# Optimization experiments

Measured on AMD Instinct MI355X. Metric: run time of the kernel, lower is better.

## Reference

```python
import jax, jax.numpy as jnp
import numpy as np

V, D, NH, L, HID, E, K = 32000, 1024, 16, 2, 2048, 8, 2
B, S = 2, 1024
HD = D // NH
EPS = 1e-6
ROPE_BASE = 10000.0


def setup_inputs() -> dict:
    key = jax.random.key(0)
    ks = jax.random.split(key, 12)
    s = 0.02
    return {
        "tokens": jax.random.randint(ks[0], (B, S), 0, V),
        "embed": jax.random.normal(ks[1], (V, D), jnp.float32) * s,
        "attn_norm_w": jnp.ones((L, D), jnp.float32),
        "wq": jax.random.normal(ks[2], (L, D, D), jnp.float32) * s,
        "wk": jax.random.normal(ks[3], (L, D, D), jnp.float32) * s,
        "wv": jax.random.normal(ks[4], (L, D, D), jnp.float32) * s,
        "wo": jax.random.normal(ks[5], (L, D, D), jnp.float32) * s,
        "moe_norm_w": jnp.ones((L, D), jnp.float32),
        "router_w": jax.random.normal(ks[6], (L, E, D), jnp.float32) * s,
        "w1": jax.random.normal(ks[7], (L, E, D, HID), jnp.float32) * s,
        "w2": jax.random.normal(ks[8], (L, E, HID, D), jnp.float32) * s,
        "w3": jax.random.normal(ks[9], (L, E, D, HID), jnp.float32) * s,
        "final_norm_w": jnp.ones((D,), jnp.float32),
    }


def rmsnorm(x, w):
    var = jnp.mean(jnp.square(x), axis=-1, keepdims=True)
    return x * jax.lax.rsqrt(var + EPS) * w


def rope(x):  # x: [B, S, NH, HD], rotate-half convention
    half = HD // 2
    inv = ROPE_BASE ** (-jnp.arange(half, dtype=jnp.float32) / half)
    ang = jnp.arange(x.shape[1], dtype=jnp.float32)[:, None] * inv[None, :]  # [S, half]
    cos = jnp.cos(ang)[None, :, None, :]
    sin = jnp.sin(ang)[None, :, None, :]
    x1, x2 = x[..., :half], x[..., half:]
    return jnp.concatenate([x1 * cos - x2 * sin, x1 * sin + x2 * cos], axis=-1)


def attention(x, wq, wk, wv, wo):
    q = (x @ wq).reshape(B, S, NH, HD)
    k = (x @ wk).reshape(B, S, NH, HD)
    v = (x @ wv).reshape(B, S, NH, HD)
    q, k = rope(q), rope(k)
    scores = jnp.einsum("bqhd,bkhd->bhqk", q, k) / jnp.sqrt(jnp.float32(HD))
    mask = jnp.tril(jnp.ones((S, S), bool))
    scores = jnp.where(mask[None, None], scores, jnp.finfo(scores.dtype).min)
    attn = jax.nn.softmax(scores, axis=-1)
    ctx = jnp.einsum("bhqk,bkhd->bqhd", attn, v).reshape(B, S, D)
    return ctx @ wo


def moe(x, router_w, w1, w2, w3):
    flat = x.reshape(-1, D)                      # [T, D]
    T = flat.shape[0]
    logits = flat @ router_w.T                   # [T, E]
    topv, topi = jax.lax.top_k(logits, K)
    topw = jax.nn.softmax(topv, axis=-1)         # softmax over selected logits
    gates = jnp.zeros((T, E), flat.dtype).at[jnp.arange(T)[:, None], topi].set(topw)
    out = jnp.zeros_like(flat)
    for e in range(E):  # small fixed expert count; gates are exact-sparse so math == dispatch path
        y = (jax.nn.silu(flat @ w1[e]) * (flat @ w3[e])) @ w2[e]
        out = out + y * gates[:, e:e + 1]
    return out.reshape(x.shape)


def reference(tokens, embed, attn_norm_w, wq, wk, wv, wo, moe_norm_w,
              router_w, w1, w2, w3, final_norm_w):
    x = embed[tokens]  # [B, S, D]
    for l in range(L):
        x = x + attention(rmsnorm(x, attn_norm_w[l]), wq[l], wk[l], wv[l], wo[l])
        x = x + moe(rmsnorm(x, moe_norm_w[l]), router_w[l], w1[l], w2[l], w3[l])
    x = rmsnorm(x, final_norm_w)
    return x @ embed.T  # tied logits [B, S, V]
```

## Files before the change

kernel.cpp:

```cpp
#include <hip/hip_runtime.h>
#include <math.h>

typedef unsigned short u16;
typedef unsigned int u32;
typedef __attribute__((ext_vector_type(8))) short bf16x8;
typedef __attribute__((ext_vector_type(4))) float f32x4;

#define TOK 2048
#define SEQ 1024
#define DM 1024
#define NEXP 8
#define VOCAB 32000
#define NL 2
#define SLOTS 5120
#define APAD 40

__device__ __forceinline__ float bf2f(u16 v) {
  u32 u = ((u32)v) << 16; float f; __builtin_memcpy(&f, &u, 4); return f;
}
__device__ __forceinline__ u16 f2bf(float f) {
  u32 u; __builtin_memcpy(&u, &f, 4);
  u += 0x7fffu + ((u >> 16) & 1u);
  return (u16)(u >> 16);
}
__device__ __forceinline__ void split8(const float* v, u16* hi, u16* lo) {
#pragma unroll
  for (int j = 0; j < 8; j++) {
    hi[j] = f2bf(v[j]);
    lo[j] = f2bf(v[j] - bf2f(hi[j]));
  }
}

__global__ __launch_bounds__(256) void k_f2bf(const float* __restrict__ in,
                                              u16* __restrict__ out, long n4) {
  long i = (long)blockIdx.x * 256 + threadIdx.x;
  long stride = (long)gridDim.x * 256;
  for (; i < n4; i += stride) {
    float4 v = ((const float4*)in)[i];
    ushort4 o;
    o.x = f2bf(v.x); o.y = f2bf(v.y); o.z = f2bf(v.z); o.w = f2bf(v.w);
    ((ushort4*)out)[i] = o;
  }
}

__device__ __forceinline__ void norm_emit_hl(float4 v, const float* __restrict__ w,
    u16* __restrict__ ohi, u16* __restrict__ olo, int t) {
  float ss = v.x * v.x + v.y * v.y + v.z * v.z + v.w * v.w;
  for (int off = 32; off; off >>= 1) ss += __shfl_xor(ss, off);
  __shared__ float red[4];
  if ((threadIdx.x & 63) == 0) red[threadIdx.x >> 6] = ss;
  __syncthreads();
  float tot = red[0] + red[1] + red[2] + red[3];
  float sc = rsqrtf(tot * (1.0f / 1024.0f) + 1e-6f);
  float4 wv = ((const float4*)w)[threadIdx.x];
  float o[4] = {v.x * sc * wv.x, v.y * sc * wv.y, v.z * sc * wv.z, v.w * sc * wv.w};
  ushort4 hi, lo;
  hi.x = f2bf(o[0]); lo.x = f2bf(o[0] - bf2f(hi.x));
  hi.y = f2bf(o[1]); lo.y = f2bf(o[1] - bf2f(hi.y));
  hi.z = f2bf(o[2]); lo.z = f2bf(o[2] - bf2f(hi.z));
  hi.w = f2bf(o[3]); lo.w = f2bf(o[3] - bf2f(hi.w));
  ((ushort4*)(ohi + (long)t * DM))[threadIdx.x] = hi;
  ((ushort4*)(olo + (long)t * DM))[threadIdx.x] = lo;
}
__device__ __forceinline__ void norm_emit_b(float4 v, const float* __restrict__ w,
    u16* __restrict__ out, int t) {
  float ss = v.x * v.x + v.y * v.y + v.z * v.z + v.w * v.w;
  for (int off = 32; off; off >>= 1) ss += __shfl_xor(ss, off);
  __shared__ float red[4];
  if ((threadIdx.x & 63) == 0) red[threadIdx.x >> 6] = ss;
  __syncthreads();
  float tot = red[0] + red[1] + red[2] + red[3];
  float sc = rsqrtf(tot * (1.0f / 1024.0f) + 1e-6f);
  float4 wv = ((const float4*)w)[threadIdx.x];
  ushort4 o;
  o.x = f2bf(v.x * sc * wv.x); o.y = f2bf(v.y * sc * wv.y);
  o.z = f2bf(v.z * sc * wv.z); o.w = f2bf(v.w * sc * wv.w);
  ((ushort4*)(out + (long)t * DM))[threadIdx.x] = o;
}

__global__ __launch_bounds__(256) void k_gather_norm(const int* __restrict__ tok,
    const float* __restrict__ embed, const float* __restrict__ w,
    float* __restrict__ x, u16* __restrict__ ohi, u16* __restrict__ olo) {
  int t = blockIdx.x;
  float4 v = ((const float4*)(embed + (long)tok[t] * DM))[threadIdx.x];
  ((float4*)(x + (long)t * DM))[threadIdx.x] = v;
  norm_emit_hl(v, w, ohi, olo, t);
}

__global__ __launch_bounds__(256) void k_rmsnorm_hl(const float* __restrict__ x,
    const float* __restrict__ w, u16* __restrict__ ohi, u16* __restrict__ olo) {
  int t = blockIdx.x;
  float4 v = ((const float4*)(x + (long)t * DM))[threadIdx.x];
  norm_emit_hl(v, w, ohi, olo, t);
}

#define KP 72
#define VP 40
#define PP 36
__global__ __launch_bounds__(256) void k_attn(const float* __restrict__ qkv,
    u16* __restrict__ chi, u16* __restrict__ clo) {
  __shared__ u16 Ksh[32 * KP], Ksl[32 * KP];
  __shared__ u16 Vsh[64 * VP], Vsl[64 * VP];
  __shared__ float Ps[4][16 * PP];
  int bid = blockIdx.x;
  int xcd = bid & 7, r = bid >> 3;
  int bh = xcd * 4 + (r >> 4);
  int qt = 15 - (r & 15);
  int b = bh >> 4, h = bh & 15;
  int tid = threadIdx.x, w = tid >> 6, lane = tid & 63;
  int lrow = lane & 15, lgrp = lane >> 4;
  int q0 = qt * 64;
  long qrow = (long)(b * SEQ + q0 + w * 16 + lrow);
  bf16x8 qh[2], ql[2];
#pragma unroll
  for (int dsl = 0; dsl < 2; dsl++) {
    const float* src = qkv + qrow * 3072 + h * 64 + dsl * 32 + lgrp * 8;
    float v[8];
    *(float4*)v = *(const float4*)src;
    *(float4*)(v + 4) = *(const float4*)(src + 4);
    u16 hi[8], lo[8];
    split8(v, hi, lo);
    qh[dsl] = *(bf16x8*)hi; ql[dsl] = *(bf16x8*)lo;
  }
  f32x4 cacc[4] = {};
  float mst[4], lst[4];
#pragma unroll
  for (int j = 0; j < 4; j++) { mst[j] = -__builtin_inff(); lst[j] = 0.0f; }
  int srow = tid >> 3, dchunk = (tid & 7) * 8;
  for (int s0 = 0; s0 < q0 + 64; s0 += 32) {
    long kvrow = (long)(b * SEQ + s0 + srow) * 3072 + h * 64;
    {
      const float* ksrc = qkv + kvrow + 1024 + dchunk;
      float v[8];
      *(float4*)v = *(const float4*)ksrc;
      *(float4*)(v + 4) = *(const float4*)(ksrc + 4);
#pragma unroll
      for (int j = 0; j < 8; j++) {
        u16 hi = f2bf(v[j]);
        Ksh[srow * KP + dchunk + j] = hi;
        Ksl[srow * KP + dchunk + j] = f2bf(v[j] - bf2f(hi));
      }
      const float* vsrc = qkv + kvrow + 2048 + dchunk;
      *(float4*)v = *(const float4*)vsrc;
      *(float4*)(v + 4) = *(const float4*)(vsrc + 4);
#pragma unroll
      for (int j = 0; j < 8; j++) {
        u16 hi = f2bf(v[j]);
        Vsh[(dchunk + j) * VP + srow] = hi;
        Vsl[(dchunk + j) * VP + srow] = f2bf(v[j] - bf2f(hi));
      }
    }
    __syncthreads();
    f32x4 sacc[2] = {};
#pragma unroll
    for (int sf = 0; sf < 2; sf++)
#pragma unroll
      for (int dsl = 0; dsl < 2; dsl++) {
        bf16x8 kh = *(const bf16x8*)(Ksh + (sf * 16 + lrow) * KP + dsl * 32 + lgrp * 8);
        bf16x8 kl = *(const bf16x8*)(Ksl + (sf * 16 + lrow) * KP + dsl * 32 + lgrp * 8);
        sacc[sf] = __builtin_amdgcn_mfma_f32_16x16x32_bf16(qh[dsl], kh, sacc[sf], 0, 0, 0);
        sacc[sf] = __builtin_amdgcn_mfma_f32_16x16x32_bf16(qh[dsl], kl, sacc[sf], 0, 0, 0);
        sacc[sf] = __builtin_amdgcn_mfma_f32_16x16x32_bf16(ql[dsl], kh, sacc[sf], 0, 0, 0);
      }
#pragma unroll
    for (int sf = 0; sf < 2; sf++)
#pragma unroll
      for (int j = 0; j < 4; j++) {
        int col = s0 + sf * 16 + lrow;
        int row = q0 + w * 16 + lgrp * 4 + j;
        float v = sacc[sf][j] * 0.125f;
        sacc[sf][j] = (col <= row) ? v : -1e30f;
      }
    float fac[4];
#pragma unroll
    for (int j = 0; j < 4; j++) {
      float mx = fmaxf(sacc[0][j], sacc[1][j]);
      for (int off = 1; off < 16; off <<= 1) mx = fmaxf(mx, __shfl_xor(mx, off));
      float mnew = fmaxf(mst[j], mx);
      float f = __expf(mst[j] - mnew);
      mst[j] = mnew;
      float p0 = __expf(sacc[0][j] - mnew);
      float p1 = __expf(sacc[1][j] - mnew);
      sacc[0][j] = p0; sacc[1][j] = p1;
      float ps = p0 + p1;
      for (int off = 1; off < 16; off <<= 1) ps += __shfl_xor(ps, off);
      lst[j] = lst[j] * f + ps;
      fac[j] = f;
    }
#pragma unroll
    for (int n = 0; n < 4; n++)
#pragma unroll
      for (int j = 0; j < 4; j++) cacc[n][j] *= fac[j];
#pragma unroll
    for (int sf = 0; sf < 2; sf++)
#pragma unroll
      for (int j = 0; j < 4; j++)
        Ps[w][(lgrp * 4 + j) * PP + sf * 16 + lrow] = sacc[sf][j];
    float pv[8];
#pragma unroll
    for (int j = 0; j < 8; j++) pv[j] = Ps[w][lrow * PP + lgrp * 8 + j];
    u16 phi[8], plo[8];
    split8(pv, phi, plo);
    bf16x8 ph = *(bf16x8*)phi, pl = *(bf16x8*)plo;
#pragma unroll
    for (int n = 0; n < 4; n++) {
      bf16x8 vh = *(const bf16x8*)(Vsh + (n * 16 + lrow) * VP + lgrp * 8);
      bf16x8 vl = *(const bf16x8*)(Vsl + (n * 16 + lrow) * VP + lgrp * 8);
      cacc[n] = __builtin_amdgcn_mfma_f32_16x16x32_bf16(ph, vh, cacc[n], 0, 0, 0);
      cacc[n] = __builtin_amdgcn_mfma_f32_16x16x32_bf16(ph, vl, cacc[n], 0, 0, 0);
      cacc[n] = __builtin_amdgcn_mfma_f32_16x16x32_bf16(pl, vh, cacc[n], 0, 0, 0);
    }
    __syncthreads();
  }
#pragma unroll
  for (int n = 0; n < 4; n++)
#pragma unroll
    for (int j = 0; j < 4; j++) {
      long t = (long)(b * SEQ + q0 + w * 16 + lgrp * 4 + j);
      float v = cacc[n][j] / lst[j];
      u16 hv = f2bf(v);
      chi[t * DM + h * 64 + n * 16 + lrow] = hv;
      clo[t * DM + h * 64 + n * 16 + lrow] = f2bf(v - bf2f(hv));
    }
}


__device__ __forceinline__ void stageB_tr(const float* __restrict__ B, int ldb,
    int k0, int n0, u16* Bh, u16* Bl, int tid, int split) {
#pragma unroll
  for (int ph = 0; ph < 2; ph++) {
    int c = tid + 256 * ph;
    int nr = c & 127;
    int ks = c >> 7;
    const float* src = B + (long)(k0 + ks * 8) * ldb + n0 + nr;
    float v[8];
#pragma unroll
    for (int j = 0; j < 8; j++) v[j] = src[(long)j * ldb];
    u16 hi[8];
#pragma unroll
    for (int j = 0; j < 8; j++) hi[j] = f2bf(v[j]);
    *(uint4*)(Bh + nr * APAD + ks * 8) = *(uint4*)hi;
    if (split) {
      u16 lo[8];
#pragma unroll
      for (int j = 0; j < 8; j++) lo[j] = f2bf(v[j] - bf2f(hi[j]));
      *(uint4*)(Bl + nr * APAD + ks * 8) = *(uint4*)lo;
    }
  }
}

__device__ __forceinline__ void stageA_cp(const u16* __restrict__ Ahi,
    const u16* __restrict__ Alo, long ldk, long m0, int k0,
    u16* Ah, u16* Al, int tid, int split) {
#pragma unroll
  for (int ph = 0; ph < 2; ph++) {
    int c = tid + 256 * ph;
    int row = c >> 2, kc = c & 3;
    long off = (m0 + row) * ldk + k0 + kc * 8;
    *(uint4*)(Ah + row * APAD + kc * 8) = *(const uint4*)(Ahi + off);
    if (split) *(uint4*)(Al + row * APAD + kc * 8) = *(const uint4*)(Alo + off);
  }
}

__global__ __launch_bounds__(256) void k_wo(
    const u16* __restrict__ Ahi, const u16* __restrict__ Alo,
    const float* __restrict__ B, float* __restrict__ C) {
  __shared__ u16 Ah[128 * APAD], Al[128 * APAD], Bh[128 * APAD], Bl[128 * APAD];
  int bid = blockIdx.x;
  int n0 = (bid & 7) * 128;
  int m0 = (bid >> 3) * 128;
  int tid = threadIdx.x, lane = tid & 63, w = tid >> 6;
  int wr = w >> 1, wc = w & 1, lrow = lane & 15, lgrp = lane >> 4;
  f32x4 acc[4][4] = {};
  for (int k0 = 0; k0 < 1024; k0 += 32) {
    stageA_cp(Ahi, Alo, DM, m0, k0, Ah, Al, tid, 1);
    stageB_tr(B, 1024, k0, n0, Bh, Bl, tid, 1);
    __syncthreads();
    bf16x8 ah[4], bh[4], al[4], bl[4];
#pragma unroll
    for (int i = 0; i < 4; i++) {
      ah[i] = *(const bf16x8*)(Ah + (wr * 64 + i * 16 + lrow) * APAD + lgrp * 8);
      al[i] = *(const bf16x8*)(Al + (wr * 64 + i * 16 + lrow) * APAD + lgrp * 8);
      bh[i] = *(const bf16x8*)(Bh + (wc * 64 + i * 16 + lrow) * APAD + lgrp * 8);
      bl[i] = *(const bf16x8*)(Bl + (wc * 64 + i * 16 + lrow) * APAD + lgrp * 8);
    }
#pragma unroll
    for (int i = 0; i < 4; i++)
#pragma unroll
      for (int j = 0; j < 4; j++) {
        acc[i][j] = __builtin_amdgcn_mfma_f32_16x16x32_bf16(ah[i], bh[j], acc[i][j], 0, 0, 0);
        acc[i][j] = __builtin_amdgcn_mfma_f32_16x16x32_bf16(ah[i], bl[j], acc[i][j], 0, 0, 0);
        acc[i][j] = __builtin_amdgcn_mfma_f32_16x16x32_bf16(al[i], bh[j], acc[i][j], 0, 0, 0);
      }
    __syncthreads();
  }
#pragma unroll
  for (int i = 0; i < 4; i++)
#pragma unroll
    for (int j = 0; j < 4; j++) {
      int col = n0 + wc * 64 + j * 16 + lrow;
#pragma unroll
      for (int jj = 0; jj < 4; jj++) {
        int r = m0 + wr * 64 + i * 16 + lgrp * 4 + jj;
        C[(long)r * DM + col] += acc[i][j][jj];
      }
    }
}

__global__ __launch_bounds__(256) void k_gemm_qkv(
    const u16* __restrict__ Ahi, const u16* __restrict__ Alo,
    const float* __restrict__ Bq, const float* __restrict__ Bk,
    const float* __restrict__ Bv, float* __restrict__ C) {
  __shared__ u16 Ah[128 * APAD], Al[128 * APAD], Bh[128 * APAD], Bl[128 * APAD];
  int bid = blockIdx.x;
  int xcd = bid & 7, r = bid >> 3;
  int nb = xcd * 3 + r / 16;
  int m0 = (r & 15) * 128;
  const float* B = (nb < 8) ? Bq : (nb < 16) ? Bk : Bv;
  int bn0 = (nb & 7) * 128;
  int tid = threadIdx.x, lane = tid & 63, w = tid >> 6;
  int wr = w >> 1, wc = w & 1, lrow = lane & 15, lgrp = lane >> 4;
  f32x4 acc[4][4] = {};
  for (int k0 = 0; k0 < 1024; k0 += 32) {
    stageA_cp(Ahi, Alo, DM, m0, k0, Ah, Al, tid, 1);
    stageB_tr(B, 1024, k0, bn0, Bh, Bl, tid, 1);
    __syncthreads();
    bf16x8 ah[4], bh[4], al[4], bl[4];
#pragma unroll
    for (int i = 0; i < 4; i++) {
      ah[i] = *(const bf16x8*)(Ah + (wr * 64 + i * 16 + lrow) * APAD + lgrp * 8);
      al[i] = *(const bf16x8*)(Al + (wr * 64 + i * 16 + lrow) * APAD + lgrp * 8);
      bh[i] = *(const bf16x8*)(Bh + (wc * 64 + i * 16 + lrow) * APAD + lgrp * 8);
      bl[i] = *(const bf16x8*)(Bl + (wc * 64 + i * 16 + lrow) * APAD + lgrp * 8);
    }
#pragma unroll
    for (int i = 0; i < 4; i++)
#pragma unroll
      for (int j = 0; j < 4; j++) {
        acc[i][j] = __builtin_amdgcn_mfma_f32_16x16x32_bf16(ah[i], bh[j], acc[i][j], 0, 0, 0);
        acc[i][j] = __builtin_amdgcn_mfma_f32_16x16x32_bf16(ah[i], bl[j], acc[i][j], 0, 0, 0);
        acc[i][j] = __builtin_amdgcn_mfma_f32_16x16x32_bf16(al[i], bh[j], acc[i][j], 0, 0, 0);
      }
    __syncthreads();
  }
  if (nb < 16) {
    float inv1 = exp2f((float)lrow * (-13.287712379549449f / 32.0f));
    float inv2 = exp2f((float)(lrow + 16) * (-13.287712379549449f / 32.0f));
#pragma unroll
    for (int i = 0; i < 4; i++)
#pragma unroll
      for (int jj = 0; jj < 4; jj++) {
        int rr = m0 + wr * 64 + i * 16 + lgrp * 4 + jj;
        float s = (float)(rr & (SEQ - 1));
        float sn1, cs1, sn2, cs2;
        sincosf(s * inv1, &sn1, &cs1);
        sincosf(s * inv2, &sn2, &cs2);
        float q1 = acc[i][0][jj], q2 = acc[i][2][jj];
        acc[i][0][jj] = q1 * cs1 - q2 * sn1;
        acc[i][2][jj] = q1 * sn1 + q2 * cs1;
        float p1 = acc[i][1][jj], p2 = acc[i][3][jj];
        acc[i][1][jj] = p1 * cs2 - p2 * sn2;
        acc[i][3][jj] = p1 * sn2 + p2 * cs2;
      }
  }
#pragma unroll
  for (int i = 0; i < 4; i++)
#pragma unroll
    for (int j = 0; j < 4; j++) {
      int col = nb * 128 + wc * 64 + j * 16 + lrow;
#pragma unroll
      for (int jj = 0; jj < 4; jj++) {
        int rr = m0 + wr * 64 + i * 16 + lgrp * 4 + jj;
        C[(long)rr * 3072 + col] = acc[i][j][jj];
      }
    }
}

template <int SPLIT>
__global__ __launch_bounds__(256) void k_w13(
    const u16* __restrict__ Ahi, const u16* __restrict__ Alo,
    const float* __restrict__ W1, const float* __restrict__ W3,
    const int* __restrict__ lists, const int* __restrict__ counts,
    const int* __restrict__ aoff,
    float* __restrict__ h13) {
  int bid = blockIdx.x;
  int xcd = bid & 7, r = bid >> 3;
  int nb = xcd * 4 + r / 40;
  int m0 = (r % 40) * 128;
  int e = -1;
#pragma unroll
  for (int i = 0; i < NEXP; i++)
    if (m0 >= aoff[i] && m0 < aoff[i + 1]) e = i;
  if (e < 0) return;
  int lr0 = m0 - aoff[e];
  int Mc = counts[e];
  if (lr0 >= Mc) return;
  const float* B = ((nb < 16) ? W1 : W3) + (size_t)e * 1024 * 2048;
  int bn0 = (nb & 15) * 128;
  const int* lst = lists + e * TOK;
  __shared__ u16 Ah[128 * APAD], Bh[128 * APAD];
  __shared__ u16 Al[SPLIT ? 128 * APAD : 1], Bl[SPLIT ? 128 * APAD : 1];
  int tid = threadIdx.x, lane = tid & 63, w = tid >> 6;
  int wr = w >> 1, wc = w & 1, lrow = lane & 15, lgrp = lane >> 4;
  f32x4 acc[4][4] = {};
  for (int k0 = 0; k0 < 1024; k0 += 32) {
#pragma unroll
    for (int ph = 0; ph < 2; ph++) {
      int c = tid + 256 * ph;
      int row = c >> 2, kc = c & 3;
      uint4 vh = make_uint4(0, 0, 0, 0), vl = make_uint4(0, 0, 0, 0);
      if (lr0 + row < Mc) {
        long off = (long)lst[lr0 + row] * DM + k0 + kc * 8;
        vh = *(const uint4*)(Ahi + off);
        if (SPLIT) vl = *(const uint4*)(Alo + off);
      }
      *(uint4*)(Ah + row * APAD + kc * 8) = vh;
      if (SPLIT) *(uint4*)(Al + row * APAD + kc * 8) = vl;
    }
    stageB_tr(B, 2048, k0, bn0, Bh, Bl, tid, SPLIT);
    __syncthreads();
    bf16x8 ah[4], bh[4];
#pragma unroll
    for (int i = 0; i < 4; i++) {
      ah[i] = *(const bf16x8*)(Ah + (wr * 64 + i * 16 + lrow) * APAD + lgrp * 8);
      bh[i] = *(const bf16x8*)(Bh + (wc * 64 + i * 16 + lrow) * APAD + lgrp * 8);
    }
#pragma unroll
    for (int i = 0; i < 4; i++)
#pragma unroll
      for (int j = 0; j < 4; j++)
        acc[i][j] = __builtin_amdgcn_mfma_f32_16x16x32_bf16(ah[i], bh[j], acc[i][j], 0, 0, 0);
    if (SPLIT) {
      bf16x8 al[4], bl[4];
#pragma unroll
      for (int i = 0; i < 4; i++) {
        al[i] = *(const bf16x8*)(Al + (wr * 64 + i * 16 + lrow) * APAD + lgrp * 8);
        bl[i] = *(const bf16x8*)(Bl + (wc * 64 + i * 16 + lrow) * APAD + lgrp * 8);
      }
#pragma unroll
      for (int i = 0; i < 4; i++)
#pragma unroll
        for (int j = 0; j < 4; j++) {
          acc[i][j] = __builtin_amdgcn_mfma_f32_16x16x32_bf16(ah[i], bl[j], acc[i][j], 0, 0, 0);
          acc[i][j] = __builtin_amdgcn_mfma_f32_16x16x32_bf16(al[i], bh[j], acc[i][j], 0, 0, 0);
        }
    }
    __syncthreads();
  }
#pragma unroll
  for (int i = 0; i < 4; i++)
#pragma unroll
    for (int j = 0; j < 4; j++) {
      int col = nb * 128 + wc * 64 + j * 16 + lrow;
#pragma unroll
      for (int jj = 0; jj < 4; jj++) {
        int rl = wr * 64 + i * 16 + lgrp * 4 + jj;
        if (lr0 + rl >= Mc) continue;
        h13[(long)(m0 + rl) * 4096 + col] = acc[i][j][jj];
      }
    }
}

__global__ __launch_bounds__(256) void k_silu(const float* __restrict__ h13,
    const int* __restrict__ counts, const int* __restrict__ aoff,
    u16* __restrict__ hhi, u16* __restrict__ hlo) {
  int g = blockIdx.x;
  int e = -1;
#pragma unroll
  for (int i = 0; i < NEXP; i++)
    if (g >= aoff[i] && g < aoff[i + 1]) e = i;
  if (e < 0 || g - aoff[e] >= counts[e]) return;
  const float4* a = (const float4*)(h13 + (long)g * 4096);
  const float4* b = (const float4*)(h13 + (long)g * 4096 + 2048);
  for (int c = threadIdx.x; c < 512; c += 256) {
    float4 x1 = a[c], x3 = b[c];
    float o[4];
    o[0] = x1.x / (1.0f + __expf(-x1.x)) * x3.x;
    o[1] = x1.y / (1.0f + __expf(-x1.y)) * x3.y;
    o[2] = x1.z / (1.0f + __expf(-x1.z)) * x3.z;
    o[3] = x1.w / (1.0f + __expf(-x1.w)) * x3.w;
    ushort4 hi, lo;
    hi.x = f2bf(o[0]); lo.x = f2bf(o[0] - bf2f(hi.x));
    hi.y = f2bf(o[1]); lo.y = f2bf(o[1] - bf2f(hi.y));
    hi.z = f2bf(o[2]); lo.z = f2bf(o[2] - bf2f(hi.z));
    hi.w = f2bf(o[3]); lo.w = f2bf(o[3] - bf2f(hi.w));
    ((ushort4*)(hhi + (long)g * 2048))[c] = hi;
    ((ushort4*)(hlo + (long)g * 2048))[c] = lo;
  }
}

template <int SPLIT>
__global__ __launch_bounds__(256) void k_w2(
    const u16* __restrict__ Ahi, const u16* __restrict__ Alo,
    const float* __restrict__ W2,
    const int* __restrict__ counts, const int* __restrict__ aoff,
    float* __restrict__ y) {
  int bid = blockIdx.x;
  int n0 = (bid & 7) * 128;
  int m0 = (bid >> 3) * 128;
  int e = -1;
#pragma unroll
  for (int i = 0; i < NEXP; i++)
    if (m0 >= aoff[i] && m0 < aoff[i + 1]) e = i;
  if (e < 0) return;
  int lr0 = m0 - aoff[e];
  int Mc = counts[e];
  if (lr0 >= Mc) return;
  const float* B = W2 + (size_t)e * 2048 * 1024;
  __shared__ u16 Ah[128 * APAD], Bh[128 * APAD];
  __shared__ u16 Al[SPLIT ? 128 * APAD : 1], Bl[SPLIT ? 128 * APAD : 1];
  int tid = threadIdx.x, lane = tid & 63, w = tid >> 6;
  int wr = w >> 1, wc = w & 1, lrow = lane & 15, lgrp = lane >> 4;
  f32x4 acc[4][4] = {};
  for (int k0 = 0; k0 < 2048; k0 += 32) {
    stageA_cp(Ahi, Alo, 2048, m0, k0, Ah, Al, tid, SPLIT);
    stageB_tr(B, 1024, k0, n0, Bh, Bl, tid, SPLIT);
    __syncthreads();
    bf16x8 ah[4], bh[4];
#pragma unroll
    for (int i = 0; i < 4; i++) {
      ah[i] = *(const bf16x8*)(Ah + (wr * 64 + i * 16 + lrow) * APAD + lgrp * 8);
      bh[i] = *(const bf16x8*)(Bh + (wc * 64 + i * 16 + lrow) * APAD + lgrp * 8);
    }
#pragma unroll
    for (int i = 0; i < 4; i++)
#pragma unroll
      for (int j = 0; j < 4; j++)
        acc[i][j] = __builtin_amdgcn_mfma_f32_16x16x32_bf16(ah[i], bh[j], acc[i][j], 0, 0, 0);
    if (SPLIT) {
      bf16x8 al[4], bl[4];
#pragma unroll
      for (int i = 0; i < 4; i++) {
        al[i] = *(const bf16x8*)(Al + (wr * 64 + i * 16 + lrow) * APAD + lgrp * 8);
        bl[i] = *(const bf16x8*)(Bl + (wc * 64 + i * 16 + lrow) * APAD + lgrp * 8);
      }
#pragma unroll
      for (int i = 0; i < 4; i++)
#pragma unroll
        for (int j = 0; j < 4; j++) {
          acc[i][j] = __builtin_amdgcn_mfma_f32_16x16x32_bf16(ah[i], bl[j], acc[i][j], 0, 0, 0);
          acc[i][j] = __builtin_amdgcn_mfma_f32_16x16x32_bf16(al[i], bh[j], acc[i][j], 0, 0, 0);
        }
    }
    __syncthreads();
  }
#pragma unroll
  for (int i = 0; i < 4; i++)
#pragma unroll
    for (int j = 0; j < 4; j++) {
      int col = n0 + wc * 64 + j * 16 + lrow;
#pragma unroll
      for (int jj = 0; jj < 4; jj++) {
        int rl = wr * 64 + i * 16 + lgrp * 4 + jj;
        if (lr0 + rl >= Mc) continue;
        y[(long)(m0 + rl) * DM + col] = acc[i][j][jj];
      }
    }
}

template <int FINAL>
__global__ __launch_bounds__(256) void k_combine_norm(const float* __restrict__ y,
    const int* __restrict__ aoff, const int* __restrict__ tok_e,
    const int* __restrict__ tok_pos, const float* __restrict__ tok_gate,
    float* __restrict__ x, const float* __restrict__ wnext,
    u16* __restrict__ ohi, u16* __restrict__ olo) {
  int t = blockIdx.x;
  float4 acc = ((float4*)(x + (long)t * DM))[threadIdx.x];
#pragma unroll
  for (int j = 0; j < 2; j++) {
    int e = tok_e[t * 2 + j];
    long g = aoff[e] + tok_pos[t * 2 + j];
    float gt = tok_gate[t * 2 + j];
    float4 yv = ((const float4*)(y + g * DM))[threadIdx.x];
    acc.x += gt * yv.x; acc.y += gt * yv.y;
    acc.z += gt * yv.z; acc.w += gt * yv.w;
  }
  ((float4*)(x + (long)t * DM))[threadIdx.x] = acc;
  if (FINAL) norm_emit_b(acc, wnext, ohi, t);
  else norm_emit_hl(acc, wnext, ohi, olo, t);
}

__device__ __forceinline__ void logits_mma(const u16* As, const u16* Bs,
    f32x4 (&acc)[4][4], int wr, int wc, int lrow, int lgrp) {
  bf16x8 af[4], bfr[4];
#pragma unroll
  for (int i = 0; i < 4; i++) {
    af[i] = *(const bf16x8*)(As + (wr * 64 + i * 16 + lrow) * APAD + lgrp * 8);
    bfr[i] = *(const bf16x8*)(Bs + (wc * 64 + i * 16 + lrow) * APAD + lgrp * 8);
  }
#pragma unroll
  for (int i = 0; i < 4; i++)
#pragma unroll
    for (int j = 0; j < 4; j++)
      acc[i][j] = __builtin_amdgcn_mfma_f32_16x16x32_bf16(af[i], bfr[j], acc[i][j], 0, 0, 0);
}

__global__ __launch_bounds__(512) void k_logits(
    const u16* __restrict__ A, const u16* __restrict__ Bt,
    float* __restrict__ C) {
  __shared__ u16 AsA[256 * APAD], BsA[128 * APAD];
  __shared__ u16 AsB[256 * APAD], BsB[128 * APAD];
  int bid = blockIdx.x;
  int xcd = bid & 7, rank = bid >> 3;
  int bx = xcd * 32 + (rank >> 3);
  int by = rank & 7;
  if (bx >= VOCAB / 128) return;
  int m0 = by * 256, n0 = bx * 128;
  int tid = threadIdx.x, lane = tid & 63, w = tid >> 6;
  int wr = w >> 1, wc = w & 1;
  int lrow = lane & 15, lgrp = lane >> 4;
  int arow = tid >> 2, akc = tid & 3;
  f32x4 acc[4][4] = {};
  const u16* Ap = A + (long)(m0 + arow) * 1024 + akc * 8;
  const u16* Ap2 = A + (long)(m0 + arow + 128) * 1024 + akc * 8;
  const u16* Bp = Bt + (long)(n0 + arow) * 1024 + akc * 8;
  uint4 a0 = *(const uint4*)(Ap);
  uint4 a1 = *(const uint4*)(Ap2);
  uint4 b0 = *(const uint4*)(Bp);
  *(uint4*)(AsA + arow * APAD + akc * 8) = a0;
  *(uint4*)(AsA + (arow + 128) * APAD + akc * 8) = a1;
  *(uint4*)(BsA + arow * APAD + akc * 8) = b0;
  __syncthreads();
  for (int kt = 0; kt < 32; kt += 2) {
    {
      int k0 = (kt + 1) * 32;
      a0 = *(const uint4*)(Ap + k0);
      a1 = *(const uint4*)(Ap2 + k0);
      b0 = *(const uint4*)(Bp + k0);
    }
    logits_mma(AsA, BsA, acc, wr, wc, lrow, lgrp);
    *(uint4*)(AsB + arow * APAD + akc * 8) = a0;
    *(uint4*)(AsB + (arow + 128) * APAD + akc * 8) = a1;
    *(uint4*)(BsB + arow * APAD + akc * 8) = b0;
    __syncthreads();
    if (kt + 2 < 32) {
      int k0 = (kt + 2) * 32;
      a0 = *(const uint4*)(Ap + k0);
      a1 = *(const uint4*)(Ap2 + k0);
      b0 = *(const uint4*)(Bp + k0);
    }
    logits_mma(AsB, BsB, acc, wr, wc, lrow, lgrp);
    if (kt + 2 < 32) {
      *(uint4*)(AsA + arow * APAD + akc * 8) = a0;
      *(uint4*)(AsA + (arow + 128) * APAD + akc * 8) = a1;
      *(uint4*)(BsA + arow * APAD + akc * 8) = b0;
    }
    __syncthreads();
  }
#pragma unroll
  for (int i = 0; i < 4; i++)
#pragma unroll
    for (int j = 0; j < 4; j++) {
      int col = n0 + wc * 64 + j * 16 + lrow;
#pragma unroll
      for (int jj = 0; jj < 4; jj++) {
        int r = m0 + wr * 64 + i * 16 + lgrp * 4 + jj;
        C[(long)r * VOCAB + col] = acc[i][j][jj];
      }
    }
}

__global__ __launch_bounds__(256) void k_router(const float* __restrict__ x,
    const float* __restrict__ nw, const float* __restrict__ rw,
    int* __restrict__ counts, int* __restrict__ lists,
    int* __restrict__ tok_e, int* __restrict__ tok_pos,
    float* __restrict__ tok_gate) {
  int t = blockIdx.x * 4 + (threadIdx.x >> 6);
  int lane = threadIdx.x & 63;
  const float* xr = x + (long)t * DM;
  float ss = 0.0f;
  float p[8] = {0, 0, 0, 0, 0, 0, 0, 0};
  for (int i = 0; i < 16; i++) {
    int d = lane + 64 * i;
    float xv = xr[d];
    ss += xv * xv;
    float xw = xv * nw[d];
#pragma unroll
    for (int e = 0; e < 8; e++) p[e] += xw * rw[e * DM + d];
  }
  for (int off = 32; off; off >>= 1) ss += __shfl_xor(ss, off);
#pragma unroll
  for (int e = 0; e < 8; e++)
    for (int off = 32; off; off >>= 1) p[e] += __shfl_xor(p[e], off);
  if (lane == 0) {
    float sc = rsqrtf(ss * (1.0f / 1024.0f) + 1e-6f);
    int e0 = 0, e1 = -1;
    float v0 = -__builtin_inff(), v1 = -__builtin_inff();
    for (int e = 0; e < 8; e++) {
      float pe = p[e] * sc;
      if (pe > v0) { v1 = v0; e1 = e0; v0 = pe; e0 = e; }
      else if (pe > v1) { v1 = pe; e1 = e; }
    }
    float w0 = 1.0f / (1.0f + expf(v1 - v0));
    int pos0 = atomicAdd(&counts[e0], 1);
    lists[e0 * TOK + pos0] = t;
    tok_e[t * 2] = e0; tok_pos[t * 2] = pos0; tok_gate[t * 2] = w0;
    int pos1 = atomicAdd(&counts[e1], 1);
    lists[e1 * TOK + pos1] = t;
    tok_e[t * 2 + 1] = e1; tok_pos[t * 2 + 1] = pos1; tok_gate[t * 2 + 1] = 1.0f - w0;
  }
}

__global__ void k_offsets(const int* __restrict__ counts, int* __restrict__ aoff) {
  if (threadIdx.x == 0 && blockIdx.x == 0) {
    int a = 0;
    for (int e = 0; e < NEXP; e++) {
      aoff[e] = a;
      a += (counts[e] + 127) & ~127;
    }
    aoff[NEXP] = a;
  }
}

extern "C" void kernel_launch(void* const* d_in, const int* in_sizes, int n_in,
                              void* d_out, int out_size, void* d_ws, size_t ws_size,
                              hipStream_t stream) {
  (void)in_sizes; (void)n_in; (void)out_size; (void)ws_size;
  const int* tokens = (const int*)d_in[0];
  const float* embed = (const float*)d_in[1];
  const float* attn_nw = (const float*)d_in[2];
  const float* wq = (const float*)d_in[3];
  const float* wk = (const float*)d_in[4];
  const float* wv = (const float*)d_in[5];
  const float* wo = (const float*)d_in[6];
  const float* moe_nw = (const float*)d_in[7];
  const float* rw = (const float*)d_in[8];
  const float* w1 = (const float*)d_in[9];
  const float* w2 = (const float*)d_in[10];
  const float* w3 = (const float*)d_in[11];
  const float* fin_nw = (const float*)d_in[12];
  float* out = (float*)d_out;

  char* ob = (char*)d_out;
  auto carve = [&](size_t bytes) { char* r = ob; ob += (bytes + 255) & ~(size_t)255; return r; };
  float* qkv    = (float*)carve((size_t)TOK * 3072 * 4);
  u16*   ctx_hi = (u16*)carve((size_t)TOK * DM * 2);
  u16*   ctx_lo = (u16*)carve((size_t)TOK * DM * 2);
  float* x      = (float*)carve((size_t)TOK * DM * 4);
  float* h13    = (float*)carve((size_t)SLOTS * 4096 * 4);
  u16*   hb_hi  = (u16*)carve((size_t)SLOTS * 2048 * 2);
  u16*   hb_lo  = (u16*)carve((size_t)SLOTS * 2048 * 2);
  float* y      = (float*)carve((size_t)SLOTS * 1024 * 4);
  int*   counts  = (int*)carve(NEXP * 4);
  int*   aoff    = (int*)carve((NEXP + 1) * 4);
  int*   lists   = (int*)carve((size_t)NEXP * TOK * 4);
  int*   tok_e   = (int*)carve((size_t)TOK * 2 * 4);
  int*   tok_pos = (int*)carve((size_t)TOK * 2 * 4);
  float* tok_gate= (float*)carve((size_t)TOK * 2 * 4);
  char* wp = (char*)d_ws;
  auto wcarve = [&](size_t bytes) { char* r = wp; wp += (bytes + 255) & ~(size_t)255; return r; };
  u16* xn_hi = (u16*)wcarve((size_t)TOK * DM * 2);
  u16* xn_lo = (u16*)wcarve((size_t)TOK * DM * 2);
  u16* xnb   = (u16*)wcarve((size_t)TOK * DM * 2);
  u16* embB  = (u16*)wcarve((size_t)VOCAB * DM * 2);

  k_f2bf<<<4096, 256, 0, stream>>>(embed, embB, (long)VOCAB * DM / 4);
  k_gather_norm<<<TOK, 256, 0, stream>>>(tokens, embed, attn_nw, x, xn_hi, xn_lo);

  for (int l = 0; l < NL; l++) {
    k_gemm_qkv<<<384, 256, 0, stream>>>(xn_hi, xn_lo,
        wq + (size_t)l * DM * DM, wk + (size_t)l * DM * DM, wv + (size_t)l * DM * DM, qkv);
    k_attn<<<512, 256, 0, stream>>>(qkv, ctx_hi, ctx_lo);
    k_wo<<<128, 256, 0, stream>>>(ctx_hi, ctx_lo, wo + (size_t)l * DM * DM, x);

    hipMemsetAsync(counts, 0, NEXP * 4, stream);
    k_router<<<TOK / 4, 256, 0, stream>>>(x, moe_nw + (size_t)l * DM,
        rw + (size_t)l * NEXP * DM, counts, lists, tok_e, tok_pos, tok_gate);
    k_offsets<<<1, 64, 0, stream>>>(counts, aoff);
    k_rmsnorm_hl<<<TOK, 256, 0, stream>>>(x, moe_nw + (size_t)l * DM, xn_hi, xn_lo);
    if (l < NL - 1) {
      k_w13<1><<<1280, 256, 0, stream>>>(xn_hi, xn_lo,
          w1 + (size_t)l * NEXP * DM * 2048, w3 + (size_t)l * NEXP * DM * 2048,
          lists, counts, aoff, h13);
      k_silu<<<SLOTS, 256, 0, stream>>>(h13, counts, aoff, hb_hi, hb_lo);
      k_w2<1><<<320, 256, 0, stream>>>(hb_hi, hb_lo,
          w2 + (size_t)l * NEXP * 2048 * DM, counts, aoff, y);
      k_combine_norm<0><<<TOK, 256, 0, stream>>>(y, aoff, tok_e, tok_pos, tok_gate,
          x, attn_nw + (size_t)(l + 1) * DM, xn_hi, xn_lo);
    } else {
      k_w13<0><<<1280, 256, 0, stream>>>(xn_hi, xn_lo,
          w1 + (size_t)l * NEXP * DM * 2048, w3 + (size_t)l * NEXP * DM * 2048,
          lists, counts, aoff, h13);
      k_silu<<<SLOTS, 256, 0, stream>>>(h13, counts, aoff, hb_hi, hb_lo);
      k_w2<0><<<320, 256, 0, stream>>>(hb_hi, hb_lo,
          w2 + (size_t)l * NEXP * 2048 * DM, counts, aoff, y);
      k_combine_norm<1><<<TOK, 256, 0, stream>>>(y, aoff, tok_e, tok_pos, tok_gate,
          x, fin_nw, xnb, nullptr);
    }
  }
  k_logits<<<2048, 512, 0, stream>>>(xnb, embB, out);
}
```

Before: 1.455 ms.

## Double-buffer last-layer MoE GEMMs and fuse MoE rmsnorm into router

Adds double-buffered versions of the expert up-projection and down-projection GEMMs, used only for the final layer's non-split bf16 path. They prefetch the next K tile into registers while the current tile's MFMAs run, with ping-pong shared-memory buffers. The MoE rmsnorm is folded into the router kernel, which now writes the hi/lo bf16 normalized activations, removing a separate kernel launch and a re-read of x. The expert-count memset is moved into the gather and combine kernels to drop a memset call, at the cost of extra shared memory and register pressure in the new GEMMs.

New measurement: 1.519 ms. 4.4% more time.

```diff
diff --git a/kernel.cpp b/kernel.cpp
--- a/kernel.cpp
+++ b/kernel.cpp
@@ -80,17 +80,12 @@
 
 __global__ __launch_bounds__(256) void k_gather_norm(const int* __restrict__ tok,
     const float* __restrict__ embed, const float* __restrict__ w,
-    float* __restrict__ x, u16* __restrict__ ohi, u16* __restrict__ olo) {
+    float* __restrict__ x, u16* __restrict__ ohi, u16* __restrict__ olo,
+    int* __restrict__ counts) {
   int t = blockIdx.x;
+  if (t == 0 && threadIdx.x < NEXP) counts[threadIdx.x] = 0;
   float4 v = ((const float4*)(embed + (long)tok[t] * DM))[threadIdx.x];
   ((float4*)(x + (long)t * DM))[threadIdx.x] = v;
-  norm_emit_hl(v, w, ohi, olo, t);
-}
-
-__global__ __launch_bounds__(256) void k_rmsnorm_hl(const float* __restrict__ x,
-    const float* __restrict__ w, u16* __restrict__ ohi, u16* __restrict__ olo) {
-  int t = blockIdx.x;
-  float4 v = ((const float4*)(x + (long)t * DM))[threadIdx.x];
   norm_emit_hl(v, w, ohi, olo, t);
 }
 
@@ -262,6 +257,35 @@
   }
 }
 
+__device__ __forceinline__ void mma1(const u16* Ah, const u16* Bh,
+    f32x4 (&acc)[4][4], int wr, int wc, int lrow, int lgrp) {
+  bf16x8 ah[4], bh[4];
+#pragma unroll
+  for (int i = 0; i < 4; i++) {
+    ah[i] = *(const bf16x8*)(Ah + (wr * 64 + i * 16 + lrow) * APAD + lgrp * 8);
+    bh[i] = *(const bf16x8*)(Bh + (wc * 64 + i * 16 + lrow) * APAD + lgrp * 8);
+  }
+#pragma unroll
+  for (int i = 0; i < 4; i++)
+#pragma unroll
+    for (int j = 0; j < 4; j++)
+      acc[i][j] = __builtin_amdgcn_mfma_f32_16x16x32_bf16(ah[i], bh[j], acc[i][j], 0, 0, 0);
+}
+__device__ __forceinline__ void wrA1(u16* Ah, int arow, int akc, uint4 h1, uint4 h2) {
+  *(uint4*)(Ah + arow * APAD + akc * 8) = h1;
+  *(uint4*)(Ah + (arow + 64) * APAD + akc * 8) = h2;
+}
+__device__ __forceinline__ void wrB1(u16* Bh, int bnr, int bks,
+    const float* v1, const float* v2) {
+  u16 hi[8];
+#pragma unroll
+  for (int j = 0; j < 8; j++) hi[j] = f2bf(v1[j]);
+  *(uint4*)(Bh + bnr * APAD + bks * 8) = *(uint4*)hi;
+#pragma unroll
+  for (int j = 0; j < 8; j++) hi[j] = f2bf(v2[j]);
+  *(uint4*)(Bh + bnr * APAD + (bks + 2) * 8) = *(uint4*)hi;
+}
+
 __global__ __launch_bounds__(256) void k_wo(
     const u16* __restrict__ Ahi, const u16* __restrict__ Alo,
     const float* __restrict__ B, float* __restrict__ C) {
@@ -444,6 +468,93 @@
           acc[i][j] = __builtin_amdgcn_mfma_f32_16x16x32_bf16(ah[i], bl[j], acc[i][j], 0, 0, 0);
           acc[i][j] = __builtin_amdgcn_mfma_f32_16x16x32_bf16(al[i], bh[j], acc[i][j], 0, 0, 0);
         }
+    }
+    __syncthreads();
+  }
+#pragma unroll
+  for (int i = 0; i < 4; i++)
+#pragma unroll
+    for (int j = 0; j < 4; j++) {
+      int col = nb * 128 + wc * 64 + j * 16 + lrow;
+#pragma unroll
+      for (int jj = 0; jj < 4; jj++) {
+        int rl = wr * 64 + i * 16 + lgrp * 4 + jj;
+        if (lr0 + rl >= Mc) continue;
+        h13[(long)(m0 + rl) * 4096 + col] = acc[i][j][jj];
+      }
+    }
+}
+
+__global__ __launch_bounds__(256) void k_w13_db(
+    const u16* __restrict__ Ahi,
+    const float* __restrict__ W1, const float* __restrict__ W3,
+    const int* __restrict__ lists, const int* __restrict__ counts,
+    const int* __restrict__ aoff, float* __restrict__ h13) {
+  int bid = blockIdx.x;
+  int xcd = bid & 7, r = bid >> 3;
+  int nb = xcd * 4 + r / 40;
+  int m0 = (r % 40) * 128;
+  int e = -1;
+#pragma unroll
+  for (int i = 0; i < NEXP; i++)
+    if (m0 >= aoff[i] && m0 < aoff[i + 1]) e = i;
+  if (e < 0) return;
+  int lr0 = m0 - aoff[e];
+  int Mc = counts[e];
+  if (lr0 >= Mc) return;
+  const float* B = ((nb < 16) ? W1 : W3) + (size_t)e * 1024 * 2048;
+  int bn0 = (nb & 15) * 128;
+  const int* lst = lists + e * TOK;
+  __shared__ u16 AhA[128 * APAD], BhA[128 * APAD];
+  __shared__ u16 AhB[128 * APAD], BhB[128 * APAD];
+  int tid = threadIdx.x, lane = tid & 63, w = tid >> 6;
+  int wr = w >> 1, wc = w & 1, lrow = lane & 15, lgrp = lane >> 4;
+  int arow = tid >> 2, akc = tid & 3;
+  int bnr = tid & 127, bks = tid >> 7;
+  long g1 = (lr0 + arow < Mc) ? (long)lst[lr0 + arow] : -1;
+  long g2 = (lr0 + arow + 64 < Mc) ? (long)lst[lr0 + arow + 64] : -1;
+  const u16* pA1 = (g1 >= 0) ? Ahi + g1 * DM + akc * 8 : nullptr;
+  const u16* pA2 = (g2 >= 0) ? Ahi + g2 * DM + akc * 8 : nullptr;
+  const float* pB1 = B + (long)(bks * 8) * 2048 + bn0 + bnr;
+  const float* pB2 = B + (long)((bks + 2) * 8) * 2048 + bn0 + bnr;
+  uint4 z = make_uint4(0, 0, 0, 0);
+  uint4 h1, h2;
+  float b1[8], b2[8];
+  f32x4 acc[4][4] = {};
+  h1 = (g1 >= 0) ? *(const uint4*)(pA1) : z;
+  h2 = (g2 >= 0) ? *(const uint4*)(pA2) : z;
+#pragma unroll
+  for (int j = 0; j < 8; j++) { b1[j] = pB1[(long)j * 2048]; b2[j] = pB2[(long)j * 2048]; }
+  wrA1(AhA, arow, akc, h1, h2);
+  wrB1(BhA, bnr, bks, b1, b2);
+  __syncthreads();
+  for (int kt = 0; kt < 32; kt += 2) {
+    {
+      int k0 = (kt + 1) * 32;
+      h1 = (g1 >= 0) ? *(const uint4*)(pA1 + k0) : z;
+      h2 = (g2 >= 0) ? *(const uint4*)(pA2 + k0) : z;
+      const float* q1 = pB1 + (long)k0 * 2048;
+      const float* q2 = pB2 + (long)k0 * 2048;
+#pragma unroll
+      for (int j = 0; j < 8; j++) { b1[j] = q1[(long)j * 2048]; b2[j] = q2[(long)j * 2048]; }
+    }
+    mma1(AhA, BhA, acc, wr, wc, lrow, lgrp);
+    wrA1(AhB, arow, akc, h1, h2);
+    wrB1(BhB, bnr, bks, b1, b2);
+    __syncthreads();
+    if (kt + 2 < 32) {
+      int k0 = (kt + 2) * 32;
+      h1 = (g1 >= 0) ? *(const uint4*)(pA1 + k0) : z;
+      h2 = (g2 >= 0) ? *(const uint4*)(pA2 + k0) : z;
+      const float* q1 = pB1 + (long)k0 * 2048;
+      const float* q2 = pB2 + (long)k0 * 2048;
+#pragma unroll
+      for (int j = 0; j < 8; j++) { b1[j] = q1[(long)j * 2048]; b2[j] = q2[(long)j * 2048]; }
+    }
+    mma1(AhB, BhB, acc, wr, wc, lrow, lgrp);
+    if (kt + 2 < 32) {
+      wrA1(AhA, arow, akc, h1, h2);
+      wrB1(BhA, bnr, bks, b1, b2);
     }
     __syncthreads();
   }
@@ -558,13 +669,94 @@
     }
 }
 
+__global__ __launch_bounds__(256) void k_w2_db(
+    const u16* __restrict__ Ahi, const float* __restrict__ W2,
+    const int* __restrict__ counts, const int* __restrict__ aoff,
+    float* __restrict__ y) {
+  int bid = blockIdx.x;
+  int n0 = (bid & 7) * 128;
+  int m0 = (bid >> 3) * 128;
+  int e = -1;
+#pragma unroll
+  for (int i = 0; i < NEXP; i++)
+    if (m0 >= aoff[i] && m0 < aoff[i + 1]) e = i;
+  if (e < 0) return;
+  int lr0 = m0 - aoff[e];
+  int Mc = counts[e];
+  if (lr0 >= Mc) return;
+  const float* B = W2 + (size_t)e * 2048 * 1024;
+  __shared__ u16 AhA[128 * APAD], BhA[128 * APAD];
+  __shared__ u16 AhB[128 * APAD], BhB[128 * APAD];
+  int tid = threadIdx.x, lane = tid & 63, w = tid >> 6;
+  int wr = w >> 1, wc = w & 1, lrow = lane & 15, lgrp = lane >> 4;
+  int arow = tid >> 2, akc = tid & 3;
+  int bnr = tid & 127, bks = tid >> 7;
+  const u16* pA1 = Ahi + (long)(m0 + arow) * 2048 + akc * 8;
+  const u16* pA2 = Ahi + (long)(m0 + arow + 64) * 2048 + akc * 8;
+  const float* pB1 = B + (long)(bks * 8) * 1024 + n0 + bnr;
+  const float* pB2 = B + (long)((bks + 2) * 8) * 1024 + n0 + bnr;
+  uint4 h1, h2;
+  float b1[8], b2[8];
+  f32x4 acc[4][4] = {};
+  h1 = *(const uint4*)(pA1);
+  h2 = *(const uint4*)(pA2);
+#pragma unroll
+  for (int j = 0; j < 8; j++) { b1[j] = pB1[(long)j * 1024]; b2[j] = pB2[(long)j * 1024]; }
+  wrA1(AhA, arow, akc, h1, h2);
+  wrB1(BhA, bnr, bks, b1, b2);
+  __syncthreads();
+  for (int kt = 0; kt < 64; kt += 2) {
+    {
+      int k0 = (kt + 1) * 32;
+      h1 = *(const uint4*)(pA1 + k0);
+      h2 = *(const uint4*)(pA2 + k0);
+      const float* q1 = pB1 + (long)k0 * 1024;
+      const float* q2 = pB2 + (long)k0 * 1024;
+#pragma unroll
+      for (int j = 0; j < 8; j++) { b1[j] = q1[(long)j * 1024]; b2[j] = q2[(long)j * 1024]; }
+    }
+    mma1(AhA, BhA, acc, wr, wc, lrow, lgrp);
+    wrA1(AhB, arow, akc, h1, h2);
+    wrB1(BhB, bnr, bks, b1, b2);
+    __syncthreads();
+    if (kt + 2 < 64) {
+      int k0 = (kt + 2) * 32;
+      h1 = *(const uint4*)(pA1 + k0);
+      h2 = *(const uint4*)(pA2 + k0);
+      const float* q1 = pB1 + (long)k0 * 1024;
+      const float* q2 = pB2 + (long)k0 * 1024;
+#pragma unroll
+      for (int j = 0; j < 8; j++) { b1[j] = q1[(long)j * 1024]; b2[j] = q2[(long)j * 1024]; }
+    }
+    mma1(AhB, BhB, acc, wr, wc, lrow, lgrp);
+    if (kt + 2 < 64) {
+      wrA1(AhA, arow, akc, h1, h2);
+      wrB1(BhA, bnr, bks, b1, b2);
+    }
+    __syncthreads();
+  }
+#pragma unroll
+  for (int i = 0; i < 4; i++)
+#pragma unroll
+    for (int j = 0; j < 4; j++) {
+      int col = n0 + wc * 64 + j * 16 + lrow;
+#pragma unroll
+      for (int jj = 0; jj < 4; jj++) {
+        int rl = wr * 64 + i * 16 + lgrp * 4 + jj;
+        if (lr0 + rl >= Mc) continue;
+        y[(long)(m0 + rl) * DM + col] = acc[i][j][jj];
+      }
+    }
+}
+
 template <int FINAL>
 __global__ __launch_bounds__(256) void k_combine_norm(const float* __restrict__ y,
     const int* __restrict__ aoff, const int* __restrict__ tok_e,
     const int* __restrict__ tok_pos, const float* __restrict__ tok_gate,
     float* __restrict__ x, const float* __restrict__ wnext,
-    u16* __restrict__ ohi, u16* __restrict__ olo) {
+    u16* __restrict__ ohi, u16* __restrict__ olo, int* __restrict__ counts) {
   int t = blockIdx.x;
+  if (!FINAL && t == 0 && threadIdx.x < NEXP) counts[threadIdx.x] = 0;
   float4 acc = ((float4*)(x + (long)t * DM))[threadIdx.x];
 #pragma unroll
   for (int j = 0; j < 2; j++) {
@@ -660,21 +852,25 @@
     }
 }
 
-__global__ __launch_bounds__(256) void k_router(const float* __restrict__ x,
+__global__ __launch_bounds__(256) void k_router_norm(const float* __restrict__ x,
     const float* __restrict__ nw, const float* __restrict__ rw,
     int* __restrict__ counts, int* __restrict__ lists,
     int* __restrict__ tok_e, int* __restrict__ tok_pos,
-    float* __restrict__ tok_gate) {
+    float* __restrict__ tok_gate,
+    u16* __restrict__ ohi, u16* __restrict__ olo) {
   int t = blockIdx.x * 4 + (threadIdx.x >> 6);
   int lane = threadIdx.x & 63;
   const float* xr = x + (long)t * DM;
+  float xv[16], wv[16];
   float ss = 0.0f;
   float p[8] = {0, 0, 0, 0, 0, 0, 0, 0};
+#pragma unroll
   for (int i = 0; i < 16; i++) {
     int d = lane + 64 * i;
-    float xv = xr[d];
-    ss += xv * xv;
-    float xw = xv * nw[d];
+    xv[i] = xr[d];
+    wv[i] = nw[d];
+    ss += xv[i] * xv[i];
+    float xw = xv[i] * wv[i];
 #pragma unroll
     for (int e = 0; e < 8; e++) p[e] += xw * rw[e * DM + d];
   }
@@ -682,8 +878,16 @@
 #pragma unroll
   for (int e = 0; e < 8; e++)
     for (int off = 32; off; off >>= 1) p[e] += __shfl_xor(p[e], off);
+  float sc = rsqrtf(ss * (1.0f / 1024.0f) + 1e-6f);
+#pragma unroll
+  for (int i = 0; i < 16; i++) {
+    int d = lane + 64 * i;
+    float o = xv[i] * sc * wv[i];
+    u16 h = f2bf(o);
+    ohi[(long)t * DM + d] = h;
+    olo[(long)t * DM + d] = f2bf(o - bf2f(h));
+  }
   if (lane == 0) {
-    float sc = rsqrtf(ss * (1.0f / 1024.0f) + 1e-6f);
     int e0 = 0, e1 = -1;
     float v0 = -__builtin_inff(), v1 = -__builtin_inff();
     for (int e = 0; e < 8; e++) {
@@ -755,7 +959,7 @@
   u16* embB  = (u16*)wcarve((size_t)VOCAB * DM * 2);
 
   k_f2bf<<<4096, 256, 0, stream>>>(embed, embB, (long)VOCAB * DM / 4);
-  k_gather_norm<<<TOK, 256, 0, stream>>>(tokens, embed, attn_nw, x, xn_hi, xn_lo);
+  k_gather_norm<<<TOK, 256, 0, stream>>>(tokens, embed, attn_nw, x, xn_hi, xn_lo, counts);
 
   for (int l = 0; l < NL; l++) {
     k_gemm_qkv<<<384, 256, 0, stream>>>(xn_hi, xn_lo,
@@ -763,11 +967,10 @@
     k_attn<<<512, 256, 0, stream>>>(qkv, ctx_hi, ctx_lo);
     k_wo<<<128, 256, 0, stream>>>(ctx_hi, ctx_lo, wo + (size_t)l * DM * DM, x);
 
-    hipMemsetAsync(counts, 0, NEXP * 4, stream);
-    k_router<<<TOK / 4, 256, 0, stream>>>(x, moe_nw + (size_t)l * DM,
-        rw + (size_t)l * NEXP * DM, counts, lists, tok_e, tok_pos, tok_gate);
+    k_router_norm<<<TOK / 4, 256, 0, stream>>>(x, moe_nw + (size_t)l * DM,
+        rw + (size_t)l * NEXP * DM, counts, lists, tok_e, tok_pos, tok_gate,
+        xn_hi, xn_lo);
     k_offsets<<<1, 64, 0, stream>>>(counts, aoff);
-    k_rmsnorm_hl<<<TOK, 256, 0, stream>>>(x, moe_nw + (size_t)l * DM, xn_hi, xn_lo);
     if (l < NL - 1) {
       k_w13<1><<<1280, 256, 0, stream>>>(xn_hi, xn_lo,
           w1 + (size_t)l * NEXP * DM * 2048, w3 + (size_t)l * NEXP * DM * 2048,
@@ -776,16 +979,16 @@
       k_w2<1><<<320, 256, 0, stream>>>(hb_hi, hb_lo,
           w2 + (size_t)l * NEXP * 2048 * DM, counts, aoff, y);
       k_combine_norm<0><<<TOK, 256, 0, stream>>>(y, aoff, tok_e, tok_pos, tok_gate,
-          x, attn_nw + (size_t)(l + 1) * DM, xn_hi, xn_lo);
+          x, attn_nw + (size_t)(l + 1) * DM, xn_hi, xn_lo, counts);
     } else {
-      k_w13<0><<<1280, 256, 0, stream>>>(xn_hi, xn_lo,
+      k_w13_db<<<1280, 256, 0, stream>>>(xn_hi,
           w1 + (size_t)l * NEXP * DM * 2048, w3 + (size_t)l * NEXP * DM * 2048,
           lists, counts, aoff, h13);
       k_silu<<<SLOTS, 256, 0, stream>>>(h13, counts, aoff, hb_hi, hb_lo);
-      k_w2<0><<<320, 256, 0, stream>>>(hb_hi, hb_lo,
+      k_w2_db<<<320, 256, 0, stream>>>(hb_hi,
           w2 + (size_t)l * NEXP * 2048 * DM, counts, aoff, y);
       k_combine_norm<1><<<TOK, 256, 0, stream>>>(y, aoff, tok_e, tok_pos, tok_gate,
-          x, fin_nw, xnb, nullptr);
+          x, fin_nw, xnb, nullptr, nullptr);
     }
   }
   k_logits<<<2048, 512, 0, stream>>>(xnb, embB, out);
```
